# Performance work log

Hardware: AMD Instinct MI355X
Metric: run time of the kernel (lower is better)

## Reference

```python
import jax, jax.numpy as jnp
import numpy as np

# ---- vocab / constraint tables (constants, derived exactly from the module's rules) ----
VOCAB = {'<pad>': 0, '<start>': 1, '<end>': 2, 'C': 3, 'O': 4, 'N': 5, '(': 6, ')': 7,
         '[': 8, ']': 9, '=': 10, '#': 11, '%': 12, '1': 13, '2': 14, '3': 15, '4': 16,
         '5': 17, '6': 18, '7': 19, '8': 20, '9': 21}
V = len(VOCAB)
CONSTRAINT_STRENGTH = 0.5

_toks = sorted(VOCAB, key=VOCAB.get)
# allowed.update(['(','[',')',']']) makes the bracket-stack branch redundant; the
# allowed set depends only on whether the previous char is a digit.
_always = {'(', ')', '[', ']', 'C', 'O', 'N', '=', '#'}
_allowed_digit = (_always | {'%'}) - {'<pad>', '<start>', '<end>'}
_allowed_nondigit = (_always | {str(i) for i in range(1, 10)}) - {'<pad>', '<start>', '<end>'}
D_DIGIT = jnp.asarray(np.array([0.0 if t in _allowed_digit else 1.0 for t in _toks], np.float32))      # [V]
D_NONDIGIT = jnp.asarray(np.array([0.0 if t in _allowed_nondigit else 1.0 for t in _toks], np.float32))  # [V]
IS_DIGIT = jnp.asarray(np.array([1.0 if t.isdigit() else 0.0 for t in _toks], np.float32))               # [V]


def setup_inputs() -> dict:
    key = jax.random.key(0)
    ks = jax.random.split(key, 5)
    B, S, D, F = 32, 512, 512, 2048
    return {
        'tokens': jax.random.randint(ks[0], (B, S), 0, V, dtype=jnp.int32),
        'z': jax.random.normal(ks[1], (B, D), dtype=jnp.float32),
        'emb': jax.random.normal(ks[2], (V, D), dtype=jnp.float32) * 0.02,
        'W1': jax.random.normal(ks[3], (D, F), dtype=jnp.float32) * 0.02,
        'b1': jnp.zeros((F,), dtype=jnp.float32),
        'W2': jax.random.normal(ks[4], (F, V), dtype=jnp.float32) * 0.02,
        'b2': jnp.zeros((V,), dtype=jnp.float32),
    }


def reference(tokens, z, emb, W1, b1, W2, b2):
    # decoder: token embedding + broadcast latent -> MLP -> logits [B,S,V]
    x = emb[tokens] + z[:, None, :]                       # [B,S,D]
    h = jax.nn.relu(jnp.einsum('bsd,df->bsf', x, W1) + b1)  # [B,S,F]
    logits = jnp.einsum('bsf,fv->bsv', h, W2) + b2          # [B,S,V]

    # constraint mask: for t in 1..S-1 add the disallowed-vector chosen by
    # whether tokens[t-1] is a digit; accumulated into one [V] mask per sequence.
    isdig = IS_DIGIT[tokens[:, :-1]]                      # [B,S-1]
    n_dig = jnp.sum(isdig, axis=1)                        # [B]
    n_non = (tokens.shape[1] - 1) - n_dig                 # [B]
    mask = n_dig[:, None] * D_DIGIT + n_non[:, None] * D_NONDIGIT  # [B,V]
    return logits - CONSTRAINT_STRENGTH * mask[:, None, :]
```

## Files before the change

### kernel.cpp

```cpp
#include <hip/hip_runtime.h>

#define V 22
#define NB 32
#define NS 512
#define ND 512
#define NF 2048
#define M_TOT 704

typedef __attribute__((ext_vector_type(8))) short bf16x8;
typedef __attribute__((ext_vector_type(4))) float f32x4;
typedef unsigned short ushort_t;

__device__ __forceinline__ unsigned short f2bf(float f) {
    unsigned u = __float_as_uint(f);
    u += 0x7FFFu + ((u >> 16) & 1u);
    return (unsigned short)(u >> 16);
}

__global__ __launch_bounds__(256) void prep_kernel(
    const int* __restrict__ tokens, const float* __restrict__ z,
    const float* __restrict__ emb, const float* __restrict__ W1,
    const float* __restrict__ b2,
    ushort_t* __restrict__ W1T, ushort_t* __restrict__ X,
    float* __restrict__ lt, int* __restrict__ n_dig)
{
    __shared__ __align__(16) unsigned short T[64 * 72];
    __shared__ int wsum[4];
    const int bid = blockIdx.x, tid = threadIdx.x;

    if (bid < 256) {
        const int k0 = (bid >> 5) * 64, f0 = (bid & 31) * 64;
        #pragma unroll
        for (int rep = 0; rep < 4; ++rep) {
            int k = rep * 16 + (tid >> 4);
            int f = (tid & 15) * 4;
            float4 v = *(const float4*)&W1[(size_t)(k0 + k) * NF + f0 + f];
            T[(f + 0) * 72 + k] = f2bf(v.x);
            T[(f + 1) * 72 + k] = f2bf(v.y);
            T[(f + 2) * 72 + k] = f2bf(v.z);
            T[(f + 3) * 72 + k] = f2bf(v.w);
        }
        __syncthreads();
        #pragma unroll
        for (int rep = 0; rep < 2; ++rep) {
            int fr = rep * 32 + (tid >> 3);
            int kc = (tid & 7) * 8;
            int4 v = *(const int4*)&T[fr * 72 + kc];
            *(int4*)&W1T[(size_t)(f0 + fr) * ND + k0 + kc] = v;
        }
    } else if (bid < 432) {
        const int g = bid - 256;
        const int r = tid >> 6;
        const int kk = (tid & 63) * 8;
        const int m = g * 4 + r;
        const int b = m / V;
        const int t = m - b * V;
        const float* er = emb + (size_t)t * ND + kk;
        const float* zr = z + (size_t)b * ND + kk;
        ushort_t o[8];
        #pragma unroll
        for (int e = 0; e < 8; ++e) o[e] = f2bf(er[e] + zr[e]);
        *(int4*)&X[(size_t)m * ND + kk] = *(int4*)o;
    } else if (bid < 464) {
        const int b = bid - 432;
        int cnt = 0;
        for (int s = tid; s < NS - 1; s += 256) {
            int t = tokens[b * NS + s];
            cnt += (t >= 13 && t <= 21);
        }
        for (int off = 32; off > 0; off >>= 1) cnt += __shfl_down(cnt, off, 64);
        if ((tid & 63) == 0) wsum[tid >> 6] = cnt;
        __syncthreads();
        if (tid == 0) n_dig[b] = wsum[0] + wsum[1] + wsum[2] + wsum[3];
    } else {
        const int i = (bid - 464) * 256 + tid;
        if (i < M_TOT * V) lt[i] = b2[i % V];
    }
}

__global__ __launch_bounds__(256) void gemm_fused(
    const ushort_t* __restrict__ X, const ushort_t* __restrict__ W1T,
    const float* __restrict__ b1, const float* __restrict__ W2,
    float* __restrict__ lt)
{
    __shared__ __align__(16) char smem[49152];
    const int tid = threadIdx.x;
    const int m0 = blockIdx.x * 32;
    const int f0 = blockIdx.y * 64;
    const int lane = tid & 63;
    const int wave = tid >> 6;
    const int wm = wave >> 1, wn = wave & 1;

    const int srow = tid >> 4;
    const int sphys = ((tid & 15) * 16) ^ ((srow & 7) << 4);
    const ushort_t* gA = X + (size_t)(m0 + srow) * ND + (tid & 15) * 8;
    const ushort_t* gB = W1T + (size_t)(f0 + srow) * ND + (tid & 15) * 8;

    const int swr = (lane & 7) << 4;
    const int rowA = wm * 16 + (lane & 15);
    const int rowB = wn * 32 + (lane & 15);
    const int kgrp = (lane >> 4) * 16;

    int4 ra0, ra1, rb0, rb1, rb2, rb3;
    f32x4 acc[2];
    acc[0] = (f32x4){0.f, 0.f, 0.f, 0.f};
    acc[1] = (f32x4){0.f, 0.f, 0.f, 0.f};

#define LOADT(kt) { \
    ra0 = *(const int4*)(gA + (kt) * 128); \
    ra1 = *(const int4*)(gA + (kt) * 128 + 16 * ND); \
    rb0 = *(const int4*)(gB + (kt) * 128); \
    rb1 = *(const int4*)(gB + (kt) * 128 + 16 * ND); \
    rb2 = *(const int4*)(gB + (kt) * 128 + 32 * ND); \
    rb3 = *(const int4*)(gB + (kt) * 128 + 48 * ND); }

#define WRITET(bufi) { \
    char* Ab = smem + (bufi) * 24576; \
    char* Bb = Ab + 8192; \
    *(int4*)(Ab + srow * 256 + sphys) = ra0; \
    *(int4*)(Ab + (srow + 16) * 256 + sphys) = ra1; \
    *(int4*)(Bb + srow * 256 + sphys) = rb0; \
    *(int4*)(Bb + (srow + 16) * 256 + sphys) = rb1; \
    *(int4*)(Bb + (srow + 32) * 256 + sphys) = rb2; \
    *(int4*)(Bb + (srow + 48) * 256 + sphys) = rb3; }

#define COMPUTET(bufi) { \
    const char* Ab = smem + (bufi) * 24576; \
    const char* Bb = Ab + 8192; \
    _Pragma("unroll") \
    for (int ks = 0; ks < 4; ++ks) { \
        int kb = ks * 64 + kgrp; \
        bf16x8 af  = *(const bf16x8*)(Ab + rowA * 256 + (kb ^ swr)); \
        bf16x8 bf0 = *(const bf16x8*)(Bb + rowB * 256 + (kb ^ swr)); \
        bf16x8 bf1 = *(const bf16x8*)(Bb + (rowB + 16) * 256 + (kb ^ swr)); \
        acc[0] = __builtin_amdgcn_mfma_f32_16x16x32_bf16(af, bf0, acc[0], 0, 0, 0); \
        acc[1] = __builtin_amdgcn_mfma_f32_16x16x32_bf16(af, bf1, acc[1], 0, 0, 0); \
    } }

    LOADT(0);              WRITET(0); __syncthreads();
    LOADT(1); COMPUTET(0); WRITET(1); __syncthreads();
    LOADT(2); COMPUTET(1); WRITET(0); __syncthreads();
    LOADT(3); COMPUTET(0); WRITET(1); __syncthreads();
              COMPUTET(1);

    float* hs  = (float*)smem;
    float* w2s = (float*)(smem + 8704);
    {
        const int mrow = wm * 16 + ((lane >> 4) << 2);
        #pragma unroll
        for (int ni = 0; ni < 2; ++ni) {
            int col = wn * 32 + ni * 16 + (lane & 15);
            float bias = b1[f0 + col];
            #pragma unroll
            for (int r = 0; r < 4; ++r)
                hs[(mrow + r) * 68 + col] = fmaxf(acc[ni][r] + bias, 0.f);
        }
    }
    for (int i = tid; i < 64 * V; i += 256) w2s[i] = W2[(size_t)f0 * V + i];
    __syncthreads();

    {
        const int row = tid >> 3;
        const int vb = (tid & 7) * 3;
        float a0 = 0.f, a1 = 0.f, a2 = 0.f;
        #pragma unroll 8
        for (int f = 0; f < 64; ++f) {
            float h = hs[row * 68 + f];
            const float* w = &w2s[f * V + vb];
            a0 = fmaf(h, w[0], a0);
            a1 = fmaf(h, w[1], a1);
            a2 = fmaf(h, w[2], a2);
        }
        float* ltr = lt + (size_t)(m0 + row) * V + vb;
        atomicAdd(ltr, a0);
        if (vb + 1 < V) atomicAdd(ltr + 1, a1);
        if (vb + 2 < V) atomicAdd(ltr + 2, a2);
    }
#undef LOADT
#undef WRITET
#undef COMPUTET
}

__global__ __launch_bounds__(256) void scatter_out(
    const int* __restrict__ tokens, const float* __restrict__ lt,
    const int* __restrict__ n_dig, float* __restrict__ out)
{
    int idx = blockIdx.x * blockDim.x + threadIdx.x;
    if (idx >= NB * NS * V) return;
    int v = idx % V;
    int bs = idx / V;
    int s = bs % NS;
    int b = bs / NS;
    int tok = tokens[b * NS + s];
    float nd = (float)n_dig[b];
    float nn = (float)(NS - 1) - nd;
    float dd = ((0x3FE007 >> v) & 1) ? 1.f : 0.f;
    float dn = ((0x001007 >> v) & 1) ? 1.f : 0.f;
    float mask = nd * dd + nn * dn;
    out[idx] = lt[(b * V + tok) * V + v] - 0.5f * mask;
}

extern "C" void kernel_launch(void* const* d_in, const int* in_sizes, int n_in,
                              void* d_out, int out_size, void* d_ws, size_t ws_size,
                              hipStream_t stream) {
    const int*   tokens = (const int*)d_in[0];
    const float* z      = (const float*)d_in[1];
    const float* emb    = (const float*)d_in[2];
    const float* W1     = (const float*)d_in[3];
    const float* b1     = (const float*)d_in[4];
    const float* W2     = (const float*)d_in[5];
    const float* b2     = (const float*)d_in[6];
    float* out = (float*)d_out;

    char* ws = (char*)d_ws;
    ushort_t* W1T = (ushort_t*)ws;
    ushort_t* X   = (ushort_t*)(ws + 2097152);
    float*    lt  = (float*)(ws + 2818048);
    int*      n_dig = (int*)(ws + 2880000);

    prep_kernel<<<525, 256, 0, stream>>>(tokens, z, emb, W1, b2, W1T, X, lt, n_dig);
    gemm_fused<<<dim3(22, 32), 256, 0, stream>>>(X, W1T, b1, W2, lt);
    scatter_out<<<1408, 256, 0, stream>>>(tokens, lt, n_dig, out);
}
```

Baseline: 87.07 us.

## Replace atomic split-F reduction with partial buffers plus combine kernel

The fused GEMM no longer atomically accumulates into the logit table. Each F-block now writes its partial logits to a separate slice, and a new combine kernel sums the 32 slices and adds b2. The digit count moves from the prep kernel into scatter_out, where every block recomputes it for its batch row. This removes atomic contention and the lt initialisation, at the cost of an extra launch, about 2 MB of partial-buffer traffic, and redundant token counting in each block.

```diff
diff --git a/kernel.cpp b/kernel.cpp
--- a/kernel.cpp
+++ b/kernel.cpp
@@ -9,23 +9,20 @@
 
 typedef __attribute__((ext_vector_type(8))) short bf16x8;
 typedef __attribute__((ext_vector_type(4))) float f32x4;
-typedef unsigned short ushort_t;
-
-__device__ __forceinline__ unsigned short f2bf(float f) {
+typedef unsigned short u16;
+
+__device__ __forceinline__ u16 f2bf(float f) {
     unsigned u = __float_as_uint(f);
     u += 0x7FFFu + ((u >> 16) & 1u);
-    return (unsigned short)(u >> 16);
+    return (u16)(u >> 16);
 }
 
 __global__ __launch_bounds__(256) void prep_kernel(
-    const int* __restrict__ tokens, const float* __restrict__ z,
-    const float* __restrict__ emb, const float* __restrict__ W1,
-    const float* __restrict__ b2,
-    ushort_t* __restrict__ W1T, ushort_t* __restrict__ X,
-    float* __restrict__ lt, int* __restrict__ n_dig)
-{
-    __shared__ __align__(16) unsigned short T[64 * 72];
-    __shared__ int wsum[4];
+    const float* __restrict__ z, const float* __restrict__ emb,
+    const float* __restrict__ W1,
+    u16* __restrict__ W1T, u16* __restrict__ X)
+{
+    __shared__ __align__(16) u16 T[64 * 72];
     const int bid = blockIdx.x, tid = threadIdx.x;
 
     if (bid < 256) {
@@ -45,10 +42,9 @@
         for (int rep = 0; rep < 2; ++rep) {
             int fr = rep * 32 + (tid >> 3);
             int kc = (tid & 7) * 8;
-            int4 v = *(const int4*)&T[fr * 72 + kc];
-            *(int4*)&W1T[(size_t)(f0 + fr) * ND + k0 + kc] = v;
-        }
-    } else if (bid < 432) {
+            *(int4*)&W1T[(size_t)(f0 + fr) * ND + k0 + kc] = *(int4*)&T[fr * 72 + kc];
+        }
+    } else {
         const int g = bid - 256;
         const int r = tid >> 6;
         const int kk = (tid & 63) * 8;
@@ -57,31 +53,17 @@
         const int t = m - b * V;
         const float* er = emb + (size_t)t * ND + kk;
         const float* zr = z + (size_t)b * ND + kk;
-        ushort_t o[8];
+        u16 o[8];
         #pragma unroll
         for (int e = 0; e < 8; ++e) o[e] = f2bf(er[e] + zr[e]);
         *(int4*)&X[(size_t)m * ND + kk] = *(int4*)o;
-    } else if (bid < 464) {
-        const int b = bid - 432;
-        int cnt = 0;
-        for (int s = tid; s < NS - 1; s += 256) {
-            int t = tokens[b * NS + s];
-            cnt += (t >= 13 && t <= 21);
-        }
-        for (int off = 32; off > 0; off >>= 1) cnt += __shfl_down(cnt, off, 64);
-        if ((tid & 63) == 0) wsum[tid >> 6] = cnt;
-        __syncthreads();
-        if (tid == 0) n_dig[b] = wsum[0] + wsum[1] + wsum[2] + wsum[3];
-    } else {
-        const int i = (bid - 464) * 256 + tid;
-        if (i < M_TOT * V) lt[i] = b2[i % V];
     }
 }
 
 __global__ __launch_bounds__(256) void gemm_fused(
-    const ushort_t* __restrict__ X, const ushort_t* __restrict__ W1T,
+    const u16* __restrict__ X, const u16* __restrict__ W1T,
     const float* __restrict__ b1, const float* __restrict__ W2,
-    float* __restrict__ lt)
+    float* __restrict__ part)
 {
     __shared__ __align__(16) char smem[49152];
     const int tid = threadIdx.x;
@@ -93,8 +75,8 @@
 
     const int srow = tid >> 4;
     const int sphys = ((tid & 15) * 16) ^ ((srow & 7) << 4);
-    const ushort_t* gA = X + (size_t)(m0 + srow) * ND + (tid & 15) * 8;
-    const ushort_t* gB = W1T + (size_t)(f0 + srow) * ND + (tid & 15) * 8;
+    const u16* gA = X + (size_t)(m0 + srow) * ND + (tid & 15) * 8;
+    const u16* gB = W1T + (size_t)(f0 + srow) * ND + (tid & 15) * 8;
 
     const int swr = (lane & 7) << 4;
     const int rowA = wm * 16 + (lane & 15);
@@ -161,7 +143,7 @@
 
     {
         const int row = tid >> 3;
-        const int vb = (tid & 7) * 3;
+        const int vb  = (tid & 7) * 3;
         float a0 = 0.f, a1 = 0.f, a2 = 0.f;
         #pragma unroll 8
         for (int f = 0; f < 64; ++f) {
@@ -171,33 +153,62 @@
             a1 = fmaf(h, w[1], a1);
             a2 = fmaf(h, w[2], a2);
         }
-        float* ltr = lt + (size_t)(m0 + row) * V + vb;
-        atomicAdd(ltr, a0);
-        if (vb + 1 < V) atomicAdd(ltr + 1, a1);
-        if (vb + 2 < V) atomicAdd(ltr + 2, a2);
+        float* pr = part + ((size_t)blockIdx.y * M_TOT + m0 + row) * V + vb;
+        pr[0] = a0;
+        if (vb + 1 < V) pr[1] = a1;
+        if (vb + 2 < V) pr[2] = a2;
     }
 #undef LOADT
 #undef WRITET
 #undef COMPUTET
 }
 
+__global__ __launch_bounds__(256) void combine(
+    const float* __restrict__ part, const float* __restrict__ b2,
+    float* __restrict__ lt)
+{
+    const int i = blockIdx.x * 256 + threadIdx.x;
+    if (i >= M_TOT * V) return;
+    float s = b2[i % V];
+    #pragma unroll
+    for (int c = 0; c < 32; ++c) s += part[c * (M_TOT * V) + i];
+    lt[i] = s;
+}
+
 __global__ __launch_bounds__(256) void scatter_out(
     const int* __restrict__ tokens, const float* __restrict__ lt,
-    const int* __restrict__ n_dig, float* __restrict__ out)
-{
-    int idx = blockIdx.x * blockDim.x + threadIdx.x;
-    if (idx >= NB * NS * V) return;
-    int v = idx % V;
-    int bs = idx / V;
-    int s = bs % NS;
-    int b = bs / NS;
-    int tok = tokens[b * NS + s];
-    float nd = (float)n_dig[b];
-    float nn = (float)(NS - 1) - nd;
-    float dd = ((0x3FE007 >> v) & 1) ? 1.f : 0.f;
-    float dn = ((0x001007 >> v) & 1) ? 1.f : 0.f;
-    float mask = nd * dd + nn * dn;
-    out[idx] = lt[(b * V + tok) * V + v] - 0.5f * mask;
+    float* __restrict__ out)
+{
+    __shared__ int wsum[4];
+    __shared__ float ndig_sh;
+    const int tid = threadIdx.x;
+    const int b = blockIdx.x / 44;
+
+    int cnt = 0;
+    {
+        int t1 = tokens[b * NS + tid];
+        cnt += (t1 >= 13 && t1 <= 21);
+        int s2 = tid + 256;
+        if (s2 < NS - 1) {
+            int t2 = tokens[b * NS + s2];
+            cnt += (t2 >= 13 && t2 <= 21);
+        }
+    }
+    for (int off = 32; off > 0; off >>= 1) cnt += __shfl_down(cnt, off, 64);
+    if ((tid & 63) == 0) wsum[tid >> 6] = cnt;
+    __syncthreads();
+    if (tid == 0) ndig_sh = (float)(wsum[0] + wsum[1] + wsum[2] + wsum[3]);
+    __syncthreads();
+
+    const int idx = blockIdx.x * 256 + tid;
+    const int v = idx % V;
+    const int s = (idx / V) & (NS - 1);
+    const int tok = tokens[b * NS + s];
+    const float nd = ndig_sh;
+    const float nn = (float)(NS - 1) - nd;
+    const float dd = ((0x3FE007 >> v) & 1) ? 1.f : 0.f;
+    const float dn = ((0x001007 >> v) & 1) ? 1.f : 0.f;
+    out[idx] = lt[((size_t)b * V + tok) * V + v] - 0.5f * (nd * dd + nn * dn);
 }
 
 extern "C" void kernel_launch(void* const* d_in, const int* in_sizes, int n_in,
@@ -213,12 +224,13 @@
     float* out = (float*)d_out;
 
     char* ws = (char*)d_ws;
-    ushort_t* W1T = (ushort_t*)ws;
-    ushort_t* X   = (ushort_t*)(ws + 2097152);
-    float*    lt  = (float*)(ws + 2818048);
-    int*      n_dig = (int*)(ws + 2880000);
-
-    prep_kernel<<<525, 256, 0, stream>>>(tokens, z, emb, W1, b2, W1T, X, lt, n_dig);
-    gemm_fused<<<dim3(22, 32), 256, 0, stream>>>(X, W1T, b1, W2, lt);
-    scatter_out<<<1408, 256, 0, stream>>>(tokens, lt, n_dig, out);
-}
+    u16*   W1T  = (u16*)ws;
+    u16*   X    = (u16*)(ws + 2097152);
+    float* part = (float*)(ws + 2818048);
+    float* lt   = (float*)(ws + 4800512);
+
+    prep_kernel<<<432, 256, 0, stream>>>(z, emb, W1, W1T, X);
+    gemm_fused<<<dim3(22, 32), 256, 0, stream>>>(X, W1T, b1, W2, part);
+    combine<<<61, 256, 0, stream>>>(part, b2, lt);
+    scatter_out<<<1408, 256, 0, stream>>>(tokens, lt, out);
+}
```

Result: no change. 87.30 us (+0.3%).
